# Performance work log

Hardware: AMD Instinct MI355X
Metric: run time of the kernel (lower is better)

Reference implementation:

```python
import jax, jax.numpy as jnp
import numpy as np

VOCAB = 32000
H = 1024          # hidden_size + 8
I = 2 * H         # gru input size
SRC = 4096

def setup_inputs() -> dict:
    key = jax.random.key(0)
    ks = jax.random.split(key, 12)
    s = 0.02
    return {
        "word_input": jax.random.randint(ks[0], (1, 1), 0, VOCAB),
        "last_context": jax.random.normal(ks[1], (1, 1, H), jnp.float32),
        "prev_hidden": jax.random.normal(ks[2], (1, 1, H), jnp.float32),
        "encoder_outputs": jax.random.normal(ks[3], (SRC, 1, H), jnp.float32),
        "emb": jax.random.normal(ks[4], (VOCAB, H), jnp.float32) * s,
        "W_ih": jax.random.normal(ks[5], (3 * H, I), jnp.float32) * s,
        "W_hh": jax.random.normal(ks[6], (3 * H, H), jnp.float32) * s,
        "b_ih": jax.random.normal(ks[7], (3 * H,), jnp.float32) * s,
        "b_hh": jax.random.normal(ks[8], (3 * H,), jnp.float32) * s,
        "W_out": jax.random.normal(ks[9], (VOCAB, I), jnp.float32) * s,
        "b_out": jax.random.normal(ks[10], (VOCAB,), jnp.float32) * s,
    }

def reference(word_input, last_context, prev_hidden, encoder_outputs,
              emb, W_ih, W_hh, b_ih, b_hh, W_out, b_out):
    # embedding lookup (dropout is identity in eval)
    x = emb[word_input.reshape(-1)[0]]                # (H,)
    rnn_in = jnp.concatenate([x, last_context[0, 0]])  # (2H,)
    h = prev_hidden[0, 0]                              # (H,)

    # single-step GRU (PyTorch gate order: r, z, n)
    gi = W_ih @ rnn_in + b_ih                          # (3H,)
    gh = W_hh @ h + b_hh                               # (3H,)
    i_r, i_z, i_n = jnp.split(gi, 3)
    h_r, h_z, h_n = jnp.split(gh, 3)
    r = jax.nn.sigmoid(i_r + h_r)
    z = jax.nn.sigmoid(i_z + h_z)
    n = jnp.tanh(i_n + r * h_n)
    h_new = (1.0 - z) * n + z * h                      # (H,)
    current_hidden = h_new.reshape(1, 1, H)

    # Luong dot attention over encoder outputs
    enc = encoder_outputs[:, 0, :]                     # (S, H)
    scores = enc @ h_new                               # (S,)
    attn_weights = jax.nn.softmax(scores).reshape(1, 1, -1)
    attn_context = (attn_weights[0] @ enc).reshape(1, 1, H)

    joined = jnp.concatenate([h_new, attn_context[0, 0]])  # (2H,)
    logits = joined @ W_out.T + b_out                  # (vocab,)
    output = jax.nn.log_softmax(logits).reshape(1, -1)
    return (output, attn_context, current_hidden, attn_weights)
```

## Files before the change

kernel.cpp:

```cpp
#include <hip/hip_runtime.h>
#include <math.h>

#define H      1024
#define I2     2048
#define G3     3072
#define SRC    4096
#define VOCAB  32000

#define OUT_CTX   32000
#define OUT_HID   33024
#define OUT_ATTW  34048

#define WS_GI     0
#define WS_GH     3072
#define WS_HNEW   6144
#define WS_SCORES 7168
#define WS_CTX    15360
#define WS_LOGITS 16384
#define WS_STATS  48384

__device__ __forceinline__ float wave_reduce_sum(float v) {
    #pragma unroll
    for (int off = 32; off > 0; off >>= 1)
        v += __shfl_down(v, off, 64);
    return v;
}

__device__ __forceinline__ float wave_reduce_max(float v) {
    #pragma unroll
    for (int off = 32; off > 0; off >>= 1)
        v = fmaxf(v, __shfl_down(v, off, 64));
    return v;
}

typedef float vfloat4 __attribute__((ext_vector_type(4)));

__device__ __forceinline__ float4 nt_load4(const float4* p) {
    vfloat4 v = __builtin_nontemporal_load((const vfloat4*)p);
    return make_float4(v.x, v.y, v.z, v.w);
}

__global__ void gru_matvec_kernel(const int* __restrict__ word,
                                  const float* __restrict__ last_ctx,
                                  const float* __restrict__ prev_h,
                                  const float* __restrict__ emb,
                                  const float* __restrict__ W_ih,
                                  const float* __restrict__ W_hh,
                                  const float* __restrict__ b_ih,
                                  const float* __restrict__ b_hh,
                                  float* __restrict__ ws) {
    __shared__ float lds[8];
    const int j = blockIdx.x;
    const int tid = threadIdx.x;
    const int w = word[0];
    const float4* emb4 = (const float4*)(emb + (long)w * H);
    const float4* ctx4 = (const float4*)last_ctx;
    const float4* h4   = (const float4*)prev_h;

    const float4* Wi = (const float4*)(W_ih + (long)j * I2);
    float gi = 0.f;
    {
        float4 wv = nt_load4(&Wi[tid]);
        float4 xv = emb4[tid];
        gi += wv.x*xv.x + wv.y*xv.y + wv.z*xv.z + wv.w*xv.w;
        wv = nt_load4(&Wi[tid + 256]);
        xv = ctx4[tid];
        gi += wv.x*xv.x + wv.y*xv.y + wv.z*xv.z + wv.w*xv.w;
    }
    const float4* Wh = (const float4*)(W_hh + (long)j * H);
    float gh;
    {
        float4 wv = nt_load4(&Wh[tid]);
        float4 hv = h4[tid];
        gh = wv.x*hv.x + wv.y*hv.y + wv.z*hv.z + wv.w*hv.w;
    }

    const int lane = tid & 63, wid = tid >> 6;
    gi = wave_reduce_sum(gi);
    gh = wave_reduce_sum(gh);
    if (lane == 0) { lds[wid] = gi; lds[4 + wid] = gh; }
    __syncthreads();
    if (tid == 0) {
        float gis = lds[0] + lds[1] + lds[2] + lds[3];
        float ghs = lds[4] + lds[5] + lds[6] + lds[7];
        ws[WS_GI + j] = gis + b_ih[j];
        ws[WS_GH + j] = ghs + b_hh[j];
    }
}

__global__ void gru_gates_kernel(const float* __restrict__ prev_h,
                                 float* __restrict__ ws,
                                 float* __restrict__ out_hid) {
    const int j = threadIdx.x;
    const float ir = ws[WS_GI + j],        hr = ws[WS_GH + j];
    const float iz = ws[WS_GI + H + j],    hz = ws[WS_GH + H + j];
    const float in_ = ws[WS_GI + 2*H + j], hn = ws[WS_GH + 2*H + j];
    const float r = 1.f / (1.f + expf(-(ir + hr)));
    const float z = 1.f / (1.f + expf(-(iz + hz)));
    const float n = tanhf(in_ + r * hn);
    const float h = prev_h[j];
    const float hnew = (1.f - z) * n + z * h;
    ws[WS_HNEW + j] = hnew;
    out_hid[j] = hnew;
    ws[WS_CTX + j] = 0.f;
}

__global__ void attn_scores_kernel(const float* __restrict__ enc,
                                   const float* __restrict__ ws_in,
                                   float* __restrict__ ws) {
    __shared__ float lds[4];
    const int s = blockIdx.x, tid = threadIdx.x;
    float4 ev = ((const float4*)(enc + (long)s * H))[tid];
    float4 hv = ((const float4*)(ws_in + WS_HNEW))[tid];
    float d = ev.x*hv.x + ev.y*hv.y + ev.z*hv.z + ev.w*hv.w;
    const int lane = tid & 63, wid = tid >> 6;
    d = wave_reduce_sum(d);
    if (lane == 0) lds[wid] = d;
    __syncthreads();
    if (tid == 0) ws[WS_SCORES + s] = lds[0] + lds[1] + lds[2] + lds[3];
}

__global__ void attn_fused_kernel(const float* __restrict__ enc,
                                  float* __restrict__ ws,
                                  float* __restrict__ out_attw) {
    __shared__ float s_e[SRC];
    __shared__ float red[4];
    __shared__ float s_stat;
    const int tid = threadIdx.x;
    const int lane = tid & 63, wid = tid >> 6;
    const float4* sc4 = (const float4*)(ws + WS_SCORES);

    float4 sv[4];
    float m = -INFINITY;
    #pragma unroll
    for (int i = 0; i < 4; ++i) {
        sv[i] = sc4[tid + 256 * i];
        m = fmaxf(m, fmaxf(fmaxf(sv[i].x, sv[i].y), fmaxf(sv[i].z, sv[i].w)));
    }
    m = wave_reduce_max(m);
    if (lane == 0) red[wid] = m;
    __syncthreads();
    if (tid == 0) s_stat = fmaxf(fmaxf(red[0], red[1]), fmaxf(red[2], red[3]));
    __syncthreads();
    const float mx = s_stat;
    float sum = 0.f;
    #pragma unroll
    for (int i = 0; i < 4; ++i) {
        float4 e;
        e.x = expf(sv[i].x - mx); e.y = expf(sv[i].y - mx);
        e.z = expf(sv[i].z - mx); e.w = expf(sv[i].w - mx);
        ((float4*)s_e)[tid + 256 * i] = e;
        sum += e.x + e.y + e.z + e.w;
    }
    sum = wave_reduce_sum(sum);
    if (lane == 0) red[wid] = sum;
    __syncthreads();
    if (tid == 0) s_stat = red[0] + red[1] + red[2] + red[3];
    __syncthreads();
    const float inv = 1.f / s_stat;

    const int s0 = blockIdx.x * 32;
    float4 acc = make_float4(0.f, 0.f, 0.f, 0.f);
    for (int s = s0; s < s0 + 32; ++s) {
        const float wgt = s_e[s] * inv;
        float4 ev = ((const float4*)(enc + (long)s * H))[tid];
        acc.x += wgt * ev.x; acc.y += wgt * ev.y;
        acc.z += wgt * ev.z; acc.w += wgt * ev.w;
    }
    float* ctx = ws + WS_CTX + tid * 4;
    atomicAdd(ctx + 0, acc.x); atomicAdd(ctx + 1, acc.y);
    atomicAdd(ctx + 2, acc.z); atomicAdd(ctx + 3, acc.w);

    if (blockIdx.x == 0) {
        #pragma unroll
        for (int i = 0; i < 4; ++i) {
            float4 e = ((float4*)s_e)[tid + 256 * i];
            float4 o = make_float4(e.x * inv, e.y * inv, e.z * inv, e.w * inv);
            ((float4*)out_attw)[tid + 256 * i] = o;
        }
    }
}

__global__ void out_proj_kernel(const float* __restrict__ W_out,
                                const float* __restrict__ b_out,
                                float* __restrict__ ws,
                                float* __restrict__ out_ctx) {
    __shared__ float4 s_j[512];
    const int tid = threadIdx.x;
    const int lane = tid & 63, wid = tid >> 6;
    s_j[tid]       = ((const float4*)(ws + WS_HNEW))[tid];
    s_j[256 + tid] = ((const float4*)(ws + WS_CTX))[tid];
    __syncthreads();

    const int vbase = blockIdx.x * 16 + wid * 4;
    #pragma unroll
    for (int rr = 0; rr < 4; ++rr) {
        const int v = vbase + rr;
        const float4* Wr = (const float4*)(W_out + (long)v * I2);
        float acc = 0.f;
        #pragma unroll
        for (int r = 0; r < 8; ++r) {
            float4 wv = nt_load4(&Wr[lane + r * 64]);
            float4 jv = s_j[lane + r * 64];
            acc += wv.x*jv.x + wv.y*jv.y + wv.z*jv.z + wv.w*jv.w;
        }
        acc = wave_reduce_sum(acc);
        if (lane == 0) ws[WS_LOGITS + v] = acc + b_out[v];
    }
    if (blockIdx.x == 0) {
        ((float4*)out_ctx)[tid] = s_j[256 + tid];
    }
}

__global__ void lse_kernel(float* __restrict__ ws) {
    __shared__ float lds[16];
    __shared__ float s_max;
    const int tid = threadIdx.x;
    const int lane = tid & 63, wid = tid >> 6;
    const float4* lg4 = (const float4*)(ws + WS_LOGITS);
    float m = -INFINITY;
    for (int i = tid; i < VOCAB / 4; i += 1024) {
        float4 v = lg4[i];
        m = fmaxf(m, fmaxf(fmaxf(v.x, v.y), fmaxf(v.z, v.w)));
    }
    m = wave_reduce_max(m);
    if (lane == 0) lds[wid] = m;
    __syncthreads();
    if (tid == 0) {
        float mm = lds[0];
        #pragma unroll
        for (int i = 1; i < 16; ++i) mm = fmaxf(mm, lds[i]);
        s_max = mm;
    }
    __syncthreads();
    const float mx = s_max;
    float s = 0.f;
    for (int i = tid; i < VOCAB / 4; i += 1024) {
        float4 v = lg4[i];
        s += expf(v.x - mx) + expf(v.y - mx) + expf(v.z - mx) + expf(v.w - mx);
    }
    s = wave_reduce_sum(s);
    if (lane == 0) lds[wid] = s;
    __syncthreads();
    if (tid == 0) {
        float t = 0.f;
        #pragma unroll
        for (int i = 0; i < 16; ++i) t += lds[i];
        ws[WS_STATS] = mx + logf(t);
    }
}

__global__ void logsoftmax_write_kernel(const float* __restrict__ ws,
                                        float* __restrict__ out) {
    const float lse = ws[WS_STATS];
    const float4* lg4 = (const float4*)(ws + WS_LOGITS);
    float4* out4 = (float4*)out;
    for (int i = blockIdx.x * 256 + threadIdx.x; i < VOCAB / 4; i += gridDim.x * 256) {
        float4 v = lg4[i];
        out4[i] = make_float4(v.x - lse, v.y - lse, v.z - lse, v.w - lse);
    }
}

extern "C" void kernel_launch(void* const* d_in, const int* in_sizes, int n_in,
                              void* d_out, int out_size, void* d_ws, size_t ws_size,
                              hipStream_t stream) {
    const int*   word     = (const int*)  d_in[0];
    const float* last_ctx = (const float*)d_in[1];
    const float* prev_h   = (const float*)d_in[2];
    const float* enc      = (const float*)d_in[3];
    const float* emb      = (const float*)d_in[4];
    const float* W_ih     = (const float*)d_in[5];
    const float* W_hh     = (const float*)d_in[6];
    const float* b_ih     = (const float*)d_in[7];
    const float* b_hh     = (const float*)d_in[8];
    const float* W_out    = (const float*)d_in[9];
    const float* b_out    = (const float*)d_in[10];
    float* out = (float*)d_out;
    float* ws  = (float*)d_ws;

    gru_matvec_kernel<<<G3, 256, 0, stream>>>(word, last_ctx, prev_h, emb,
                                              W_ih, W_hh, b_ih, b_hh, ws);
    gru_gates_kernel<<<1, 1024, 0, stream>>>(prev_h, ws, out + OUT_HID);
    attn_scores_kernel<<<SRC, 256, 0, stream>>>(enc, ws, ws);
    attn_fused_kernel<<<128, 256, 0, stream>>>(enc, ws, out + OUT_ATTW);
    out_proj_kernel<<<VOCAB / 16, 256, 0, stream>>>(W_out, b_out, ws, out + OUT_CTX);
    lse_kernel<<<1, 1024, 0, stream>>>(ws);
    logsoftmax_write_kernel<<<32, 256, 0, stream>>>(ws, out);
}
```

Before: 455.7 us.

## Overlap attention context with h-half of output projection; fuse LSE and write

The output projection is split into two halves. The half that uses h_new now runs in the same launch as the attention-context blocks, so W_out streaming overlaps the softmax and context reduction. A separate kernel then adds the context half plus bias into the logits. The log-sum-exp and log-softmax write are merged into one single-block kernel that keeps the logits in registers, removing a launch and a second read. The cost is an extra read-modify-write of the logits and a heterogeneous grid with branch divergence between block types.

```diff
diff --git a/kernel.cpp b/kernel.cpp
--- a/kernel.cpp
+++ b/kernel.cpp
@@ -17,7 +17,9 @@
 #define WS_SCORES 7168
 #define WS_CTX    15360
 #define WS_LOGITS 16384
-#define WS_STATS  48384
+
+#define NATT   128
+#define NPROJ  2000
 
 __device__ __forceinline__ float wave_reduce_sum(float v) {
     #pragma unroll
@@ -120,108 +122,136 @@
     if (tid == 0) ws[WS_SCORES + s] = lds[0] + lds[1] + lds[2] + lds[3];
 }
 
-__global__ void attn_fused_kernel(const float* __restrict__ enc,
+__global__ void attn_projh_kernel(const float* __restrict__ enc,
+                                  const float* __restrict__ W_out,
                                   float* __restrict__ ws,
                                   float* __restrict__ out_attw) {
-    __shared__ float s_e[SRC];
+    __shared__ float smem[SRC];
     __shared__ float red[4];
     __shared__ float s_stat;
     const int tid = threadIdx.x;
     const int lane = tid & 63, wid = tid >> 6;
-    const float4* sc4 = (const float4*)(ws + WS_SCORES);
-
-    float4 sv[4];
-    float m = -INFINITY;
-    #pragma unroll
-    for (int i = 0; i < 4; ++i) {
-        sv[i] = sc4[tid + 256 * i];
-        m = fmaxf(m, fmaxf(fmaxf(sv[i].x, sv[i].y), fmaxf(sv[i].z, sv[i].w)));
-    }
-    m = wave_reduce_max(m);
-    if (lane == 0) red[wid] = m;
-    __syncthreads();
-    if (tid == 0) s_stat = fmaxf(fmaxf(red[0], red[1]), fmaxf(red[2], red[3]));
-    __syncthreads();
-    const float mx = s_stat;
-    float sum = 0.f;
-    #pragma unroll
-    for (int i = 0; i < 4; ++i) {
-        float4 e;
-        e.x = expf(sv[i].x - mx); e.y = expf(sv[i].y - mx);
-        e.z = expf(sv[i].z - mx); e.w = expf(sv[i].w - mx);
-        ((float4*)s_e)[tid + 256 * i] = e;
-        sum += e.x + e.y + e.z + e.w;
-    }
-    sum = wave_reduce_sum(sum);
-    if (lane == 0) red[wid] = sum;
-    __syncthreads();
-    if (tid == 0) s_stat = red[0] + red[1] + red[2] + red[3];
-    __syncthreads();
-    const float inv = 1.f / s_stat;
-
-    const int s0 = blockIdx.x * 32;
-    float4 acc = make_float4(0.f, 0.f, 0.f, 0.f);
-    for (int s = s0; s < s0 + 32; ++s) {
-        const float wgt = s_e[s] * inv;
-        float4 ev = ((const float4*)(enc + (long)s * H))[tid];
-        acc.x += wgt * ev.x; acc.y += wgt * ev.y;
-        acc.z += wgt * ev.z; acc.w += wgt * ev.w;
-    }
-    float* ctx = ws + WS_CTX + tid * 4;
-    atomicAdd(ctx + 0, acc.x); atomicAdd(ctx + 1, acc.y);
-    atomicAdd(ctx + 2, acc.z); atomicAdd(ctx + 3, acc.w);
-
-    if (blockIdx.x == 0) {
+
+    if (blockIdx.x < NATT) {
+        const float4* sc4 = (const float4*)(ws + WS_SCORES);
+        float4 sv[4];
+        float m = -INFINITY;
         #pragma unroll
         for (int i = 0; i < 4; ++i) {
-            float4 e = ((float4*)s_e)[tid + 256 * i];
-            float4 o = make_float4(e.x * inv, e.y * inv, e.z * inv, e.w * inv);
-            ((float4*)out_attw)[tid + 256 * i] = o;
-        }
-    }
-}
-
-__global__ void out_proj_kernel(const float* __restrict__ W_out,
-                                const float* __restrict__ b_out,
-                                float* __restrict__ ws,
-                                float* __restrict__ out_ctx) {
-    __shared__ float4 s_j[512];
+            sv[i] = sc4[tid + 256 * i];
+            m = fmaxf(m, fmaxf(fmaxf(sv[i].x, sv[i].y), fmaxf(sv[i].z, sv[i].w)));
+        }
+        m = wave_reduce_max(m);
+        if (lane == 0) red[wid] = m;
+        __syncthreads();
+        if (tid == 0) s_stat = fmaxf(fmaxf(red[0], red[1]), fmaxf(red[2], red[3]));
+        __syncthreads();
+        const float mx = s_stat;
+        float sum = 0.f;
+        #pragma unroll
+        for (int i = 0; i < 4; ++i) {
+            float4 e;
+            e.x = expf(sv[i].x - mx); e.y = expf(sv[i].y - mx);
+            e.z = expf(sv[i].z - mx); e.w = expf(sv[i].w - mx);
+            ((float4*)smem)[tid + 256 * i] = e;
+            sum += e.x + e.y + e.z + e.w;
+        }
+        sum = wave_reduce_sum(sum);
+        if (lane == 0) red[wid] = sum;
+        __syncthreads();
+        if (tid == 0) s_stat = red[0] + red[1] + red[2] + red[3];
+        __syncthreads();
+        const float inv = 1.f / s_stat;
+
+        const int s0 = blockIdx.x * (SRC / NATT);
+        float4 acc = make_float4(0.f, 0.f, 0.f, 0.f);
+        for (int s = s0; s < s0 + SRC / NATT; ++s) {
+            const float wgt = smem[s] * inv;
+            float4 ev = ((const float4*)(enc + (long)s * H))[tid];
+            acc.x += wgt * ev.x; acc.y += wgt * ev.y;
+            acc.z += wgt * ev.z; acc.w += wgt * ev.w;
+        }
+        float* ctx = ws + WS_CTX + tid * 4;
+        atomicAdd(ctx + 0, acc.x); atomicAdd(ctx + 1, acc.y);
+        atomicAdd(ctx + 2, acc.z); atomicAdd(ctx + 3, acc.w);
+
+        if (blockIdx.x == 0) {
+            #pragma unroll
+            for (int i = 0; i < 4; ++i) {
+                float4 e = ((float4*)smem)[tid + 256 * i];
+                ((float4*)out_attw)[tid + 256 * i] =
+                    make_float4(e.x * inv, e.y * inv, e.z * inv, e.w * inv);
+            }
+        }
+    } else {
+        float4* s_h4 = (float4*)smem;
+        s_h4[tid] = ((const float4*)(ws + WS_HNEW))[tid];
+        __syncthreads();
+        const int pb = blockIdx.x - NATT;
+        const int vbase = pb * 16 + wid * 4;
+        #pragma unroll
+        for (int rr = 0; rr < 4; ++rr) {
+            const int v = vbase + rr;
+            const float4* Wr = (const float4*)(W_out + (long)v * I2);
+            float acc = 0.f;
+            #pragma unroll
+            for (int r = 0; r < 4; ++r) {
+                float4 wv = nt_load4(&Wr[lane + r * 64]);
+                float4 jv = s_h4[lane + r * 64];
+                acc += wv.x*jv.x + wv.y*jv.y + wv.z*jv.z + wv.w*jv.w;
+            }
+            acc = wave_reduce_sum(acc);
+            if (lane == 0) ws[WS_LOGITS + v] = acc;
+        }
+    }
+}
+
+__global__ void projc_kernel(const float* __restrict__ W_out,
+                             const float* __restrict__ b_out,
+                             float* __restrict__ ws,
+                             float* __restrict__ out_ctx) {
+    __shared__ float4 s_c4[256];
     const int tid = threadIdx.x;
     const int lane = tid & 63, wid = tid >> 6;
-    s_j[tid]       = ((const float4*)(ws + WS_HNEW))[tid];
-    s_j[256 + tid] = ((const float4*)(ws + WS_CTX))[tid];
-    __syncthreads();
-
+    s_c4[tid] = ((const float4*)(ws + WS_CTX))[tid];
+    __syncthreads();
     const int vbase = blockIdx.x * 16 + wid * 4;
     #pragma unroll
     for (int rr = 0; rr < 4; ++rr) {
         const int v = vbase + rr;
-        const float4* Wr = (const float4*)(W_out + (long)v * I2);
+        const float4* Wr = (const float4*)(W_out + (long)v * I2 + H);
         float acc = 0.f;
         #pragma unroll
-        for (int r = 0; r < 8; ++r) {
+        for (int r = 0; r < 4; ++r) {
             float4 wv = nt_load4(&Wr[lane + r * 64]);
-            float4 jv = s_j[lane + r * 64];
+            float4 jv = s_c4[lane + r * 64];
             acc += wv.x*jv.x + wv.y*jv.y + wv.z*jv.z + wv.w*jv.w;
         }
         acc = wave_reduce_sum(acc);
-        if (lane == 0) ws[WS_LOGITS + v] = acc + b_out[v];
+        if (lane == 0) ws[WS_LOGITS + v] += acc + b_out[v];
     }
     if (blockIdx.x == 0) {
-        ((float4*)out_ctx)[tid] = s_j[256 + tid];
-    }
-}
-
-__global__ void lse_kernel(float* __restrict__ ws) {
+        ((float4*)out_ctx)[tid] = s_c4[tid];
+    }
+}
+
+__global__ void lse_write_kernel(const float* __restrict__ ws,
+                                 float* __restrict__ out) {
     __shared__ float lds[16];
-    __shared__ float s_max;
+    __shared__ float s_bcast;
     const int tid = threadIdx.x;
     const int lane = tid & 63, wid = tid >> 6;
     const float4* lg4 = (const float4*)(ws + WS_LOGITS);
+
+    float4 v[8];
     float m = -INFINITY;
-    for (int i = tid; i < VOCAB / 4; i += 1024) {
-        float4 v = lg4[i];
-        m = fmaxf(m, fmaxf(fmaxf(v.x, v.y), fmaxf(v.z, v.w)));
+    #pragma unroll
+    for (int i = 0; i < 8; ++i) {
+        const int idx = tid + i * 1024;
+        if (idx < VOCAB / 4) {
+            v[i] = lg4[idx];
+            m = fmaxf(m, fmaxf(fmaxf(v[i].x, v[i].y), fmaxf(v[i].z, v[i].w)));
+        }
     }
     m = wave_reduce_max(m);
     if (lane == 0) lds[wid] = m;
@@ -230,14 +260,17 @@
         float mm = lds[0];
         #pragma unroll
         for (int i = 1; i < 16; ++i) mm = fmaxf(mm, lds[i]);
-        s_max = mm;
-    }
-    __syncthreads();
-    const float mx = s_max;
+        s_bcast = mm;
+    }
+    __syncthreads();
+    const float mx = s_bcast;
     float s = 0.f;
-    for (int i = tid; i < VOCAB / 4; i += 1024) {
-        float4 v = lg4[i];
-        s += expf(v.x - mx) + expf(v.y - mx) + expf(v.z - mx) + expf(v.w - mx);
+    #pragma unroll
+    for (int i = 0; i < 8; ++i) {
+        const int idx = tid + i * 1024;
+        if (idx < VOCAB / 4)
+            s += expf(v[i].x - mx) + expf(v[i].y - mx)
+               + expf(v[i].z - mx) + expf(v[i].w - mx);
     }
     s = wave_reduce_sum(s);
     if (lane == 0) lds[wid] = s;
@@ -246,18 +279,17 @@
         float t = 0.f;
         #pragma unroll
         for (int i = 0; i < 16; ++i) t += lds[i];
-        ws[WS_STATS] = mx + logf(t);
-    }
-}
-
-__global__ void logsoftmax_write_kernel(const float* __restrict__ ws,
-                                        float* __restrict__ out) {
-    const float lse = ws[WS_STATS];
-    const float4* lg4 = (const float4*)(ws + WS_LOGITS);
+        s_bcast = mx + logf(t);
+    }
+    __syncthreads();
+    const float lse = s_bcast;
     float4* out4 = (float4*)out;
-    for (int i = blockIdx.x * 256 + threadIdx.x; i < VOCAB / 4; i += gridDim.x * 256) {
-        float4 v = lg4[i];
-        out4[i] = make_float4(v.x - lse, v.y - lse, v.z - lse, v.w - lse);
+    #pragma unroll
+    for (int i = 0; i < 8; ++i) {
+        const int idx = tid + i * 1024;
+        if (idx < VOCAB / 4)
+            out4[idx] = make_float4(v[i].x - lse, v[i].y - lse,
+                                    v[i].z - lse, v[i].w - lse);
     }
 }
 
@@ -282,8 +314,7 @@
                                               W_ih, W_hh, b_ih, b_hh, ws);
     gru_gates_kernel<<<1, 1024, 0, stream>>>(prev_h, ws, out + OUT_HID);
     attn_scores_kernel<<<SRC, 256, 0, stream>>>(enc, ws, ws);
-    attn_fused_kernel<<<128, 256, 0, stream>>>(enc, ws, out + OUT_ATTW);
-    out_proj_kernel<<<VOCAB / 16, 256, 0, stream>>>(W_out, b_out, ws, out + OUT_CTX);
-    lse_kernel<<<1, 1024, 0, stream>>>(ws);
-    logsoftmax_write_kernel<<<32, 256, 0, stream>>>(ws, out);
-}
+    attn_projh_kernel<<<NATT + NPROJ, 256, 0, stream>>>(enc, W_out, ws, out + OUT_ATTW);
+    projc_kernel<<<NPROJ, 256, 0, stream>>>(W_out, b_out, ws, out + OUT_CTX);
+    lse_write_kernel<<<1, 1024, 0, stream>>>(ws, out);
+}
```

Result: no change. 455.7 us (+0.0%).
